# Performance work log

Hardware: AMD Instinct MI355X
Metric: run time of the kernel (lower is better)

## Reference

```python
import jax, jax.numpy as jnp
import numpy as np

N = 10000      # nodes
ND = 64        # node_dim
H = 128        # hidden_dim
L = 4          # num_layers
K = 16         # knn k
TD = 16        # time_dim


def _time_embed(t, n):
    # sinusoidal embedding, matches _time_embed: freqs = exp(linspace(0,1,half)*-4)
    half = TD // 2
    freqs = jnp.exp(jnp.linspace(0.0, 1.0, half) * -4.0)            # [half]
    angles = t.reshape(1, 1) * freqs[None, :]                        # [1, half]
    emb = jnp.concatenate([jnp.sin(angles), jnp.cos(angles)], -1)    # [1, TD]
    return jnp.broadcast_to(emb, (n, TD))


def _knn_edges(pos, k):
    # full cdist + topk, mirroring _knn_graph (no_grad in torch)
    n = pos.shape[0]
    sq = jnp.sum(pos * pos, -1)
    d2 = sq[:, None] + sq[None, :] - 2.0 * (pos @ pos.T)             # [N, N]
    idxr = jnp.arange(n)
    d2 = d2.at[idxr, idxr].set(jnp.inf)
    _, nbr = jax.lax.top_k(-d2, k)                                   # [N, K] nearest
    src = jnp.repeat(idxr, k)
    dst = nbr.reshape(-1)
    return src, dst


def _egnn_layer(h, pos, src, dst, s, ew1, eb1, ew2, eb2, nw1, nb1, nw2, nb2, cw, cb):
    n = h.shape[0]
    diff = pos[dst] - pos[src]                                       # [E, 3]
    r2 = jnp.sum(diff * diff, -1, keepdims=True)                     # [E, 1]
    r = jnp.sqrt(r2 + 1e-8)
    dir_ij = diff / r
    e_in = jnp.concatenate([h[dst], h[src], r2], -1)                 # [E, 2H+1]
    m = jax.nn.silu(e_in @ ew1 + eb1)
    m = jax.nn.silu(m @ ew2 + eb2)                                   # [E, H]
    m = m * s[src][:, None]                                          # s-gate
    m_sum = jax.ops.segment_sum(m, dst, num_segments=n)              # [N, H]
    deg = jax.ops.segment_sum(jnp.ones((m.shape[0], 1), m.dtype), dst, num_segments=n)
    deg = jnp.maximum(deg, 1.0)
    m_sum = m_sum / deg
    hn = jax.nn.silu(jnp.concatenate([h, m_sum], -1) @ nw1 + nb1)
    h_new = hn @ nw2 + nb2                                           # [N, H]
    gamma = m @ cw + cb                                              # [E, 1]
    cu = jax.ops.segment_sum(gamma * dir_ij, dst, num_segments=n) / deg
    return h_new, pos + cu


def setup_inputs() -> dict:
    key = jax.random.key(0)
    ks = jax.random.split(key, 24)
    g = lambda k, shape: (jax.random.normal(k, shape, dtype=jnp.float32) * 0.05)
    z = lambda shape: jnp.zeros(shape, jnp.float32)
    return {
        'x': jax.random.normal(ks[0], (N, ND), jnp.float32),
        'pos': jax.random.normal(ks[1], (N, 3), jnp.float32) * 5.0,
        't': jax.random.uniform(ks[2], (1,), jnp.float32),
        's': jax.random.uniform(ks[3], (N,), jnp.float32),
        'proj_w': g(ks[4], (ND + 1 + TD, H)), 'proj_b': z((H,)),
        'edge_w1': g(ks[5], (L, 2 * H + 1, H)), 'edge_b1': z((L, H)),
        'edge_w2': g(ks[6], (L, H, H)), 'edge_b2': z((L, H)),
        'node_w1': g(ks[7], (L, 2 * H, H)), 'node_b1': z((L, H)),
        'node_w2': g(ks[8], (L, H, H)), 'node_b2': z((L, H)),
        'coord_w': g(ks[9], (L, H, 1)), 'coord_b': z((L, 1)),
        'ec_w': g(ks[10], (H, 3)), 'ec_b': z((3,)),
        'ef_w': g(ks[11], (H, ND)), 'ef_b': z((ND,)),
    }


def reference(x, pos, t, s, proj_w, proj_b, edge_w1, edge_b1, edge_w2, edge_b2,
              node_w1, node_b1, node_w2, node_b2, coord_w, coord_b,
              ec_w, ec_b, ef_w, ef_b):
    n = x.shape[0]
    src, dst = _knn_edges(jax.lax.stop_gradient(pos), K)  # graph build is no_grad
    temb = _time_embed(t[0], n)
    h = jnp.concatenate([x, s[:, None], temb], -1) @ proj_w + proj_b  # [N, H]
    p = pos
    for l in range(L):
        h, p = _egnn_layer(h, p, src, dst, s,
                           edge_w1[l], edge_b1[l], edge_w2[l], edge_b2[l],
                           node_w1[l], node_b1[l], node_w2[l], node_b2[l],
                           coord_w[l], coord_b[l])
    eps_c = h @ ec_w + ec_b                                           # [N, 3]
    eps_f = h @ ef_w + ef_b                                           # [N, ND]
    return jnp.concatenate([eps_c, eps_f, p], -1)                     # [N, 3+ND+3]
```

## Files before the change

kernel.cpp:

```cpp
#include <hip/hip_runtime.h>
#include <math.h>

#define N_NODES 10000
#define ND 64
#define H 128
#define LAYERS 4
#define KNN 16
#define TD 16
#define E_EDGES (N_NODES * KNN)
#define KC 1250
#define TILE_E 128

typedef __attribute__((ext_vector_type(8))) short short8;
typedef __attribute__((ext_vector_type(4))) float f32x4;

__device__ __forceinline__ float silu(float x) {
  return x * __builtin_amdgcn_rcpf(1.0f + __expf(-x));
}

__device__ __forceinline__ unsigned short f2bf(float f) {
  unsigned int u = __float_as_uint(f);
  u += 0x7fffu + ((u >> 16) & 1u);
  return (unsigned short)(u >> 16);
}
__device__ __forceinline__ float bf2f(unsigned short h) {
  return __uint_as_float(((unsigned int)h) << 16);
}

__global__ __launch_bounds__(256) void pos4_kernel(const float* __restrict__ pos,
                                                   float4* __restrict__ pos4,
                                                   float* __restrict__ p0,
                                                   int* __restrict__ degi) {
  int i = blockIdx.x * 256 + threadIdx.x;
  if (i >= N_NODES) return;
  float x = pos[i * 3 + 0], y = pos[i * 3 + 1], z = pos[i * 3 + 2];
  pos4[i] = make_float4(x, y, z, x * x + y * y + z * z);
  p0[i * 3 + 0] = x;
  p0[i * 3 + 1] = y;
  p0[i * 3 + 2] = z;
  degi[i] = 0;
}

__global__ __launch_bounds__(256) void wcvt_kernel(
    const float* __restrict__ ew2, const float* __restrict__ nw1,
    const float* __restrict__ nw2, const float* __restrict__ ew1,
    const float* __restrict__ pw, const float* __restrict__ ecw,
    const float* __restrict__ efw, unsigned short* __restrict__ w2T,
    unsigned short* __restrict__ nw1T, unsigned short* __restrict__ nw2T,
    unsigned short* __restrict__ ew1T, unsigned short* __restrict__ pwT,
    unsigned short* __restrict__ owT) {
  int i = blockIdx.x * 256 + threadIdx.x;
  if (i < 65536) {
    int l = i >> 14, rem = i & 16383, o = rem >> 7, c = rem & 127;
    w2T[i] = f2bf(ew2[l * 16384 + c * 128 + o]);
  } else if (i < 196608) {
    int j = i - 65536;
    int l = j >> 15, rem = j & 32767, o = rem >> 8, c2 = rem & 255;
    nw1T[j] = f2bf(nw1[l * 32768 + c2 * 128 + o]);
  } else if (i < 262144) {
    int j = i - 196608;
    int l = j >> 14, rem = j & 16383, o = rem >> 7, c = rem & 127;
    nw2T[j] = f2bf(nw2[l * 16384 + c * 128 + o]);
  } else if (i < 393216) {
    int j = i - 262144;
    int l = j >> 15, rem = j & 32767, o = rem >> 7, c = rem & 127;
    ew1T[j] = f2bf(ew1[l * 257 * 128 + (c + ((o >> 7) << 7)) * 128 + (o & 127)]);
  } else if (i < 405504) {
    int j = i - 393216;
    int o = j / 96, c = j - o * 96;
    pwT[j] = (c < 81) ? f2bf(pw[c * 128 + o]) : 0;
  } else {
    int j = i - 405504;
    int o = j >> 7, c = j & 127;
    float v = 0.0f;
    if (o < 3) v = ecw[c * 3 + o];
    else if (o < 67) v = efw[c * 64 + (o - 3)];
    owT[j] = f2bf(v);
  }
}

__global__ __launch_bounds__(256) void knn_kernel(const float4* __restrict__ pos4,
                                                  int* __restrict__ nbr,
                                                  int* __restrict__ degi) {
  __shared__ float4 C[KC];
  int tid = threadIdx.x;
  int lane = tid & 63;
  int wid = tid >> 6;
  int i = blockIdx.x * 4 + wid;
  float4 q = pos4[i];
  float v = __builtin_inff();
  int vid = 0;
  float thresh = __builtin_inff();
  for (int base = 0; base < N_NODES; base += KC) {
    int cnt = min(KC, N_NODES - base);
    __syncthreads();
    for (int jj = tid; jj < cnt; jj += 256) C[jj] = pos4[base + jj];
    __syncthreads();
    for (int j0 = 0; j0 < cnt; j0 += 128) {
      int ja = j0 + lane, jb = j0 + 64 + lane;
      float da = __builtin_inff(), db = __builtin_inff();
      if (ja < cnt) {
        float4 p = C[ja];
        float dot = fmaf(q.x, p.x, fmaf(q.y, p.y, q.z * p.z));
        da = fmaf(-2.0f, dot, p.w);
        if (base + ja == i) da = __builtin_inff();
      }
      if (jb < cnt) {
        float4 p = C[jb];
        float dot = fmaf(q.x, p.x, fmaf(q.y, p.y, q.z * p.z));
        db = fmaf(-2.0f, dot, p.w);
        if (base + jb == i) db = __builtin_inff();
      }
      if (__ballot(fminf(da, db) < thresh)) {
        unsigned long long mask = __ballot(da < thresh);
        while (mask) {
          int sl = __ffsll((long long)mask) - 1;
          mask &= mask - 1;
          float d2b = __shfl(da, sl, 64);
          if (d2b >= thresh) continue;
          int gjb = base + j0 + sl;
          float prevv = __shfl_up(v, 1, 64);
          int previd = __shfl_up(vid, 1, 64);
          bool stay = (v <= d2b);
          bool takenew = (lane == 0) || (prevv <= d2b);
          v = stay ? v : (takenew ? d2b : prevv);
          vid = stay ? vid : (takenew ? gjb : previd);
          thresh = __shfl(v, 15, 64);
        }
        mask = __ballot(db < thresh);
        while (mask) {
          int sl = __ffsll((long long)mask) - 1;
          mask &= mask - 1;
          float d2b = __shfl(db, sl, 64);
          if (d2b >= thresh) continue;
          int gjb = base + j0 + 64 + sl;
          float prevv = __shfl_up(v, 1, 64);
          int previd = __shfl_up(vid, 1, 64);
          bool stay = (v <= d2b);
          bool takenew = (lane == 0) || (prevv <= d2b);
          v = stay ? v : (takenew ? d2b : prevv);
          vid = stay ? vid : (takenew ? gjb : previd);
          thresh = __shfl(v, 15, 64);
        }
      }
    }
  }
  if (lane < KNN) {
    nbr[i * KNN + lane] = vid;
    atomicAdd(&degi[vid], 1);
  }
}

__global__ __launch_bounds__(1024) void scan_kernel(const int* __restrict__ degi,
                                                    int* __restrict__ off,
                                                    int* __restrict__ cursor) {
  __shared__ int part[1024];
  int t = threadIdx.x;
  int base = t * 10;
  int sum = 0;
  if (t < 1000)
    for (int i = 0; i < 10; ++i) sum += degi[base + i];
  part[t] = sum;
  __syncthreads();
  for (int stp = 1; stp < 1024; stp <<= 1) {
    int v = (t >= stp) ? part[t - stp] : 0;
    __syncthreads();
    part[t] += v;
    __syncthreads();
  }
  if (t < 1000) {
    int run = (t == 0) ? 0 : part[t - 1];
    for (int i = 0; i < 10; ++i) {
      off[base + i] = run;
      cursor[base + i] = run;
      run += degi[base + i];
    }
  }
  if (t == 0) off[N_NODES] = E_EDGES;
}

__global__ void scatter_kernel(const int* __restrict__ nbr, int* __restrict__ cursor,
                               int* __restrict__ eid, int* __restrict__ dstof) {
  int e = blockIdx.x * 256 + threadIdx.x;
  if (e < E_EDGES) {
    int d = nbr[e];
    int p = atomicAdd(&cursor[d], 1);
    eid[p] = e;
    dstof[p] = d;
  }
}

__global__ void sort_kernel(const int* __restrict__ off, int* __restrict__ eid) {
  int n = blockIdx.x * 256 + threadIdx.x;
  if (n >= N_NODES) return;
  int a = off[n], b = off[n + 1];
  for (int i = a + 1; i < b; ++i) {
    int v = eid[i];
    int j = i - 1;
    while (j >= a && eid[j] > v) { eid[j + 1] = eid[j]; --j; }
    eid[j + 1] = v;
  }
}

__global__ __launch_bounds__(256) void proj_ab_kernel(
    const float* __restrict__ x, const float* __restrict__ s,
    const float* __restrict__ tptr, const unsigned short* __restrict__ pwT,
    const float* __restrict__ pb, const unsigned short* __restrict__ ew1T,
    const float* __restrict__ eb1, float* __restrict__ h_out,
    unsigned short* __restrict__ Abf, unsigned short* __restrict__ Bbf) {
  __shared__ unsigned short inpb[16][104];
  __shared__ unsigned short hb[16][136];
  int tid = threadIdx.x;
  int n0 = blockIdx.x * 16;
  float t = tptr[0];
  for (int idx = tid; idx < 16 * 104; idx += 256) {
    int n = idx / 104, c = idx - n * 104;
    int gn = n0 + n;
    float val;
    if (c < 64) val = x[gn * ND + c];
    else if (c == 64) val = s[gn];
    else if (c < 81) {
      int j = c - 65;
      int jj = (j < 8) ? j : (j - 8);
      float f = __expf(-4.0f * (float)jj / 7.0f);
      float a = t * f;
      val = (j < 8) ? sinf(a) : cosf(a);
    } else val = 0.0f;
    inpb[n][c] = f2bf(val);
  }
  __syncthreads();
  int w = tid >> 6, lane = tid & 63, fr = lane & 15, kg = lane >> 4;
  f32x4 acc[2];
  acc[0] = (f32x4){0.f, 0.f, 0.f, 0.f};
  acc[1] = (f32x4){0.f, 0.f, 0.f, 0.f};
#pragma unroll
  for (int ks = 0; ks < 3; ++ks) {
    int k = ks * 32 + kg * 8;
    short8 a = *(const short8*)&inpb[fr][k];
#pragma unroll
    for (int nt = 0; nt < 2; ++nt) {
      int col = w * 32 + nt * 16 + fr;
      short8 b = *(const short8*)&pwT[col * 96 + k];
      acc[nt] = __builtin_amdgcn_mfma_f32_16x16x32_bf16(a, b, acc[nt], 0, 0, 0);
    }
  }
#pragma unroll
  for (int nt = 0; nt < 2; ++nt) {
    int col = w * 32 + nt * 16 + fr;
    float bias = pb[col];
#pragma unroll
    for (int r = 0; r < 4; ++r) {
      int row = kg * 4 + r;
      float hv = acc[nt][r] + bias;
      h_out[(n0 + row) * H + col] = hv;
      hb[row][col] = f2bf(hv);
    }
  }
  __syncthreads();
  f32x4 acc2[4];
#pragma unroll
  for (int nt = 0; nt < 4; ++nt) acc2[nt] = (f32x4){0.f, 0.f, 0.f, 0.f};
#pragma unroll
  for (int ks = 0; ks < 4; ++ks) {
    int k = ks * 32 + kg * 8;
    short8 a = *(const short8*)&hb[fr][k];
#pragma unroll
    for (int nt = 0; nt < 4; ++nt) {
      int col = w * 64 + nt * 16 + fr;
      short8 b = *(const short8*)&ew1T[col * H + k];
      acc2[nt] = __builtin_amdgcn_mfma_f32_16x16x32_bf16(a, b, acc2[nt], 0, 0, 0);
    }
  }
#pragma unroll
  for (int nt = 0; nt < 4; ++nt) {
    int col = w * 64 + nt * 16 + fr;
    float bias = (col < H) ? eb1[col] : 0.0f;
#pragma unroll
    for (int r = 0; r < 4; ++r) {
      int row = kg * 4 + r;
      float val = acc2[nt][r] + bias;
      if (col < H) Abf[(n0 + row) * H + col] = f2bf(val);
      else Bbf[(n0 + row) * H + (col - H)] = f2bf(val);
    }
  }
}

__global__ __launch_bounds__(256) void edge_mfma_kernel(
    const unsigned short* __restrict__ Abf, const unsigned short* __restrict__ Bbf,
    const float* __restrict__ p, const float* __restrict__ s,
    const int* __restrict__ csr_off, const int* __restrict__ eid,
    const int* __restrict__ dstof, const float* __restrict__ wr,
    const unsigned short* __restrict__ w2T, const float* __restrict__ eb2,
    const float* __restrict__ cw, const float* __restrict__ cbp,
    float* __restrict__ msA, float* __restrict__ msB,
    float* __restrict__ cuA, float* __restrict__ cuB) {
  __shared__ unsigned short t1s[TILE_E][136];
  __shared__ float r2A[TILE_E], sA[TILE_E], dirA[TILE_E][3], gA[TILE_E];
  __shared__ int srcA[TILE_E], dstA[TILE_E];
  __shared__ float wrs[H], b2s[H], cws[H];

  int tid = threadIdx.x;
  int P0 = blockIdx.x * TILE_E;
  int P1 = P0 + TILE_E;

  if (tid < H) { wrs[tid] = wr[tid]; b2s[tid] = eb2[tid]; cws[tid] = cw[tid]; }
  if (tid < TILE_E) {
    int e = tid;
    int edge = eid[P0 + e];
    int src = edge >> 4;
    int d = dstof[P0 + e];
    srcA[e] = src;
    dstA[e] = d;
    float dx = p[d * 3 + 0] - p[src * 3 + 0];
    float dy = p[d * 3 + 1] - p[src * 3 + 1];
    float dz = p[d * 3 + 2] - p[src * 3 + 2];
    float r2 = dx * dx + dy * dy + dz * dz;
    r2A[e] = r2;
    float rinv = 1.0f / sqrtf(r2 + 1e-8f);
    dirA[e][0] = dx * rinv;
    dirA[e][1] = dy * rinv;
    dirA[e][2] = dz * rinv;
    sA[e] = s[src];
  }
  __syncthreads();

  int nA = dstA[0], nB = dstA[TILE_E - 1];
  int nn = nB - nA + 1;

  for (int idx = tid; idx < TILE_E * 32; idx += 256) {
    int e = idx >> 5, cp = (idx & 31) * 4;
    uint2 au = *(const uint2*)&Abf[dstA[e] * H + cp];
    uint2 bu = *(const uint2*)&Bbf[srcA[e] * H + cp];
    float r2v = r2A[e];
    float pr0 = silu(bf2f((unsigned short)(au.x & 0xffffu)) +
                     bf2f((unsigned short)(bu.x & 0xffffu)) + r2v * wrs[cp]);
    float pr1 = silu(bf2f((unsigned short)(au.x >> 16)) +
                     bf2f((unsigned short)(bu.x >> 16)) + r2v * wrs[cp + 1]);
    float pr2 = silu(bf2f((unsigned short)(au.y & 0xffffu)) +
                     bf2f((unsigned short)(bu.y & 0xffffu)) + r2v * wrs[cp + 2]);
    float pr3 = silu(bf2f((unsigned short)(au.y >> 16)) +
                     bf2f((unsigned short)(bu.y >> 16)) + r2v * wrs[cp + 3]);
    uint2 o;
    o.x = ((unsigned int)f2bf(pr1) << 16) | (unsigned int)f2bf(pr0);
    o.y = ((unsigned int)f2bf(pr3) << 16) | (unsigned int)f2bf(pr2);
    *(uint2*)&t1s[e][cp] = o;
  }
  __syncthreads();

  int w = tid >> 6, lane = tid & 63;
  int fr = lane & 15, kg = lane >> 4;
  f32x4 acc[8][2];
#pragma unroll
  for (int mt = 0; mt < 8; ++mt)
#pragma unroll
    for (int nt = 0; nt < 2; ++nt) acc[mt][nt] = (f32x4){0.f, 0.f, 0.f, 0.f};
#pragma unroll
  for (int ks = 0; ks < 4; ++ks) {
    int k = ks * 32 + kg * 8;
    short8 bf0 = *(const short8*)&w2T[(w * 32 + fr) * H + k];
    short8 bf1 = *(const short8*)&w2T[(w * 32 + 16 + fr) * H + k];
#pragma unroll
    for (int mt = 0; mt < 8; ++mt) {
      short8 a = *(const short8*)&t1s[mt * 16 + fr][k];
      acc[mt][0] = __builtin_amdgcn_mfma_f32_16x16x32_bf16(a, bf0, acc[mt][0], 0, 0, 0);
      acc[mt][1] = __builtin_amdgcn_mfma_f32_16x16x32_bf16(a, bf1, acc[mt][1], 0, 0, 0);
    }
  }
  __syncthreads();

#pragma unroll
  for (int mt = 0; mt < 8; ++mt) {
#pragma unroll
    for (int nt = 0; nt < 2; ++nt) {
      int col = w * 32 + nt * 16 + fr;
      float b2v = b2s[col];
#pragma unroll
      for (int r = 0; r < 4; ++r) {
        int row = mt * 16 + kg * 4 + r;
        float mv = silu(acc[mt][nt][r] + b2v) * sA[row];
        t1s[row][col] = f2bf(mv);
      }
    }
  }
  __syncthreads();

  if (tid < TILE_E) {
    float g = 0.f;
    for (int c = 0; c < H; c += 4) {
      uint2 u = *(const uint2*)&t1s[tid][c];
      g = fmaf(bf2f((unsigned short)(u.x & 0xffffu)), cws[c], g);
      g = fmaf(bf2f((unsigned short)(u.x >> 16)), cws[c + 1], g);
      g = fmaf(bf2f((unsigned short)(u.y & 0xffffu)), cws[c + 2], g);
      g = fmaf(bf2f((unsigned short)(u.y >> 16)), cws[c + 3], g);
    }
    gA[tid] = g + cbp[0];
  }
  __syncthreads();

  for (int idx = tid; idx < nn * H; idx += 256) {
    int ni = idx >> 7, c = idx & 127;
    int n = nA + ni;
    int o0 = csr_off[n], o1 = csr_off[n + 1];
    int lo = max(o0, P0), hi = min(o1, P1);
    float sum = 0.f;
    for (int pos = lo; pos < hi; ++pos) sum += bf2f(t1s[pos - P0][c]);
    if (o0 >= P0) {
      msA[n * H + c] = sum;
      if (o1 <= P1) msB[n * H + c] = 0.0f;
    } else {
      msB[n * H + c] = sum;
    }
  }
  for (int idx = tid; idx < nn * 3; idx += 256) {
    int ni = idx / 3, comp = idx - ni * 3;
    int n = nA + ni;
    int o0 = csr_off[n], o1 = csr_off[n + 1];
    int lo = max(o0, P0), hi = min(o1, P1);
    float sum = 0.f;
    for (int pos = lo; pos < hi; ++pos)
      sum += gA[pos - P0] * dirA[pos - P0][comp];
    if (o0 >= P0) {
      cuA[n * 3 + comp] = sum;
      if (o1 <= P1) cuB[n * 3 + comp] = 0.0f;
    } else {
      cuB[n * 3 + comp] = sum;
    }
  }
}

__global__ __launch_bounds__(256) void node_mfma_kernel(
    const float* __restrict__ h, const float* __restrict__ msA,
    const float* __restrict__ msB, const int* __restrict__ degi,
    const float* __restrict__ cuA, const float* __restrict__ cuB,
    const float* __restrict__ p_in, const unsigned short* __restrict__ w1T,
    const float* __restrict__ nb1, const unsigned short* __restrict__ w2T,
    const float* __restrict__ nb2, const unsigned short* __restrict__ ew1Tn,
    const float* __restrict__ eb1n, int doab, float* __restrict__ h_out,
    float* __restrict__ p_out, unsigned short* __restrict__ Abf,
    unsigned short* __restrict__ Bbf) {
  __shared__ unsigned short insb[16][264];
  __shared__ unsigned short hnsb[16][136];
  int tid = threadIdx.x;
  int n0 = blockIdx.x * 16;
  for (int idx = tid; idx < 16 * H; idx += 256) {
    int n = idx >> 7, c = idx & 127;
    int gn = n0 + n;
    float hv = h[gn * H + c];
    int dg = degi[gn];
    float ms = 0.f;
    if (dg > 0) ms = (msA[gn * H + c] + msB[gn * H + c]) / (float)dg;
    insb[n][c] = f2bf(hv);
    insb[n][H + c] = f2bf(ms);
  }
  __syncthreads();
  int w = tid >> 6, lane = tid & 63, fr = lane & 15, kg = lane >> 4;
  f32x4 acc[2];
  acc[0] = (f32x4){0.f, 0.f, 0.f, 0.f};
  acc[1] = (f32x4){0.f, 0.f, 0.f, 0.f};
#pragma unroll
  for (int ks = 0; ks < 8; ++ks) {
    int k = ks * 32 + kg * 8;
    short8 a = *(const short8*)&insb[fr][k];
#pragma unroll
    for (int nt = 0; nt < 2; ++nt) {
      int col = w * 32 + nt * 16 + fr;
      short8 b = *(const short8*)&w1T[col * 256 + k];
      acc[nt] = __builtin_amdgcn_mfma_f32_16x16x32_bf16(a, b, acc[nt], 0, 0, 0);
    }
  }
#pragma unroll
  for (int nt = 0; nt < 2; ++nt) {
    int col = w * 32 + nt * 16 + fr;
    float b1 = nb1[col];
#pragma unroll
    for (int r = 0; r < 4; ++r) {
      int row = kg * 4 + r;
      hnsb[row][col] = f2bf(silu(acc[nt][r] + b1));
    }
  }
  __syncthreads();
  f32x4 acc2[2];
  acc2[0] = (f32x4){0.f, 0.f, 0.f, 0.f};
  acc2[1] = (f32x4){0.f, 0.f, 0.f, 0.f};
#pragma unroll
  for (int ks = 0; ks < 4; ++ks) {
    int k = ks * 32 + kg * 8;
    short8 a = *(const short8*)&hnsb[fr][k];
#pragma unroll
    for (int nt = 0; nt < 2; ++nt) {
      int col = w * 32 + nt * 16 + fr;
      short8 b = *(const short8*)&w2T[col * H + k];
      acc2[nt] = __builtin_amdgcn_mfma_f32_16x16x32_bf16(a, b, acc2[nt], 0, 0, 0);
    }
  }
  unsigned short (*hb)[136] = (unsigned short(*)[136])insb;
#pragma unroll
  for (int nt = 0; nt < 2; ++nt) {
    int col = w * 32 + nt * 16 + fr;
    float b2 = nb2[col];
#pragma unroll
    for (int r = 0; r < 4; ++r) {
      int row = kg * 4 + r;
      float hv = acc2[nt][r] + b2;
      h_out[(n0 + row) * H + col] = hv;
      hb[row][col] = f2bf(hv);
    }
  }
  if (tid < 48) {
    int nl = tid / 3, comp = tid - nl * 3;
    int gn = n0 + nl;
    int dg = degi[gn];
    float add = 0.0f;
    if (dg > 0)
      add = (cuA[gn * 3 + comp] + cuB[gn * 3 + comp]) / (float)dg;
    p_out[gn * 3 + comp] = p_in[gn * 3 + comp] + add;
  }
  if (doab) {
    __syncthreads();
    f32x4 acc3[4];
#pragma unroll
    for (int nt = 0; nt < 4; ++nt) acc3[nt] = (f32x4){0.f, 0.f, 0.f, 0.f};
#pragma unroll
    for (int ks = 0; ks < 4; ++ks) {
      int k = ks * 32 + kg * 8;
      short8 a = *(const short8*)&hb[fr][k];
#pragma unroll
      for (int nt = 0; nt < 4; ++nt) {
        int col = w * 64 + nt * 16 + fr;
        short8 b = *(const short8*)&ew1Tn[col * H + k];
        acc3[nt] = __builtin_amdgcn_mfma_f32_16x16x32_bf16(a, b, acc3[nt], 0, 0, 0);
      }
    }
#pragma unroll
    for (int nt = 0; nt < 4; ++nt) {
      int col = w * 64 + nt * 16 + fr;
      float bias = (col < H) ? eb1n[col] : 0.0f;
#pragma unroll
      for (int r = 0; r < 4; ++r) {
        int row = kg * 4 + r;
        float val = acc3[nt][r] + bias;
        if (col < H) Abf[(n0 + row) * H + col] = f2bf(val);
        else Bbf[(n0 + row) * H + (col - H)] = f2bf(val);
      }
    }
  }
}

__global__ __launch_bounds__(256) void out_mfma_kernel(
    const float* __restrict__ h, const float* __restrict__ p,
    const unsigned short* __restrict__ owT, const float* __restrict__ ecb,
    const float* __restrict__ efb, float* __restrict__ out) {
  __shared__ unsigned short hb[16][136];
  int tid = threadIdx.x;
  int n0 = blockIdx.x * 16;
  for (int idx = tid; idx < 16 * H; idx += 256) {
    int n = idx >> 7, c = idx & 127;
    hb[n][c] = f2bf(h[(n0 + n) * H + c]);
  }
  __syncthreads();
  int w = tid >> 6, lane = tid & 63, fr = lane & 15, kg = lane >> 4;
  int ntiles = (w == 0) ? 2 : 1;
  for (int tt = 0; tt < ntiles; ++tt) {
    int tile = (tt == 0) ? w : 4;
    f32x4 acc = (f32x4){0.f, 0.f, 0.f, 0.f};
    int col = tile * 16 + fr;
#pragma unroll
    for (int ks = 0; ks < 4; ++ks) {
      int k = ks * 32 + kg * 8;
      short8 a = *(const short8*)&hb[fr][k];
      short8 b = *(const short8*)&owT[col * H + k];
      acc = __builtin_amdgcn_mfma_f32_16x16x32_bf16(a, b, acc, 0, 0, 0);
    }
    if (col < 67) {
      float bias = (col < 3) ? ecb[col] : efb[col - 3];
#pragma unroll
      for (int r = 0; r < 4; ++r) {
        int row = kg * 4 + r;
        out[(n0 + row) * 70 + col] = acc[r] + bias;
      }
    }
  }
  if (tid < 48) {
    int nl = tid / 3, comp = tid - nl * 3;
    int gn = n0 + nl;
    out[gn * 70 + 67 + comp] = p[gn * 3 + comp];
  }
}

extern "C" void kernel_launch(void* const* d_in, const int* in_sizes, int n_in,
                              void* d_out, int out_size, void* d_ws, size_t ws_size,
                              hipStream_t stream) {
  const float* x = (const float*)d_in[0];
  const float* pos = (const float*)d_in[1];
  const float* t = (const float*)d_in[2];
  const float* s = (const float*)d_in[3];
  const float* pw = (const float*)d_in[4];
  const float* pb = (const float*)d_in[5];
  const float* ew1 = (const float*)d_in[6];
  const float* eb1 = (const float*)d_in[7];
  const float* ew2 = (const float*)d_in[8];
  const float* eb2 = (const float*)d_in[9];
  const float* nw1 = (const float*)d_in[10];
  const float* nb1 = (const float*)d_in[11];
  const float* nw2 = (const float*)d_in[12];
  const float* nb2 = (const float*)d_in[13];
  const float* cw = (const float*)d_in[14];
  const float* cb = (const float*)d_in[15];
  const float* ecw = (const float*)d_in[16];
  const float* ecb = (const float*)d_in[17];
  const float* efw = (const float*)d_in[18];
  const float* efb = (const float*)d_in[19];

  char* wp = (char*)d_ws;
  auto alloc = [&](size_t bytes) {
    char* r = wp;
    wp += (bytes + 255) & ~(size_t)255;
    return r;
  };
  float* h0 = (float*)alloc((size_t)N_NODES * H * 4);
  float* h1 = (float*)alloc((size_t)N_NODES * H * 4);
  unsigned short* Abf = (unsigned short*)alloc((size_t)N_NODES * H * 2);
  unsigned short* Bbf = (unsigned short*)alloc((size_t)N_NODES * H * 2);
  float* msAb = (float*)alloc((size_t)N_NODES * H * 4);
  float* msBb = (float*)alloc((size_t)N_NODES * H * 4);
  float* cuAb = (float*)alloc((size_t)N_NODES * 3 * 4);
  float* cuBb = (float*)alloc((size_t)N_NODES * 3 * 4);
  float* p0 = (float*)alloc((size_t)N_NODES * 3 * 4);
  float* p1 = (float*)alloc((size_t)N_NODES * 3 * 4);
  int* degi = (int*)alloc((size_t)N_NODES * 4);
  int* nbr = (int*)alloc((size_t)E_EDGES * 4);
  int* off = (int*)alloc((size_t)(N_NODES + 1) * 4);
  int* cursor = (int*)alloc((size_t)N_NODES * 4);
  int* eid = (int*)alloc((size_t)E_EDGES * 4);
  int* dstof = (int*)alloc((size_t)E_EDGES * 4);
  unsigned short* w2Tb = (unsigned short*)alloc((size_t)LAYERS * H * H * 2);
  unsigned short* nw1Tb = (unsigned short*)alloc((size_t)LAYERS * 2 * H * H * 2);
  unsigned short* nw2Tb = (unsigned short*)alloc((size_t)LAYERS * H * H * 2);
  unsigned short* ew1Tb = (unsigned short*)alloc((size_t)LAYERS * 2 * H * H * 2);
  unsigned short* pwTb = (unsigned short*)alloc((size_t)H * 96 * 2);
  unsigned short* owTb = (unsigned short*)alloc((size_t)80 * H * 2);

  float4* pos4 = (float4*)msAb;

  wcvt_kernel<<<1624, 256, 0, stream>>>(ew2, nw1, nw2, ew1, pw, ecw, efw,
                                        w2Tb, nw1Tb, nw2Tb, ew1Tb, pwTb, owTb);
  pos4_kernel<<<(N_NODES + 255) / 256, 256, 0, stream>>>(pos, pos4, p0, degi);
  knn_kernel<<<N_NODES / 4, 256, 0, stream>>>(pos4, nbr, degi);
  scan_kernel<<<1, 1024, 0, stream>>>(degi, off, cursor);
  scatter_kernel<<<(E_EDGES + 255) / 256, 256, 0, stream>>>(nbr, cursor, eid, dstof);
  sort_kernel<<<(N_NODES + 255) / 256, 256, 0, stream>>>(off, eid);
  proj_ab_kernel<<<N_NODES / 16, 256, 0, stream>>>(x, s, t, pwTb, pb, ew1Tb, eb1,
                                                   h0, Abf, Bbf);

  float* hc = h0;
  float* hn = h1;
  float* pc = p0;
  float* pn = p1;
  for (int l = 0; l < LAYERS; ++l) {
    const float* ew1l = ew1 + (size_t)l * 257 * H;
    int doab = (l < LAYERS - 1) ? 1 : 0;
    edge_mfma_kernel<<<E_EDGES / TILE_E, 256, 0, stream>>>(
        Abf, Bbf, pc, s, off, eid, dstof, ew1l + 256 * H,
        w2Tb + (size_t)l * H * H, eb2 + l * H, cw + l * H, cb + l,
        msAb, msBb, cuAb, cuBb);
    node_mfma_kernel<<<N_NODES / 16, 256, 0, stream>>>(
        hc, msAb, msBb, degi, cuAb, cuBb, pc, nw1Tb + (size_t)l * 2 * H * H,
        nb1 + l * H, nw2Tb + (size_t)l * H * H, nb2 + l * H,
        ew1Tb + (size_t)(l + doab) * 2 * H * H, eb1 + (size_t)(l + doab) * H,
        doab, hn, pn, Abf, Bbf);
    float* tmp = hc; hc = hn; hn = tmp;
    tmp = pc; pc = pn; pn = tmp;
  }
  out_mfma_kernel<<<N_NODES / 16, 256, 0, stream>>>(hc, pc, owTb, ecb, efb,
                                                    (float*)d_out);
}
```

Before: 450.7 us.

## Process two queries per wave in kNN, coalesce weight transpose, vectorize edge reductions

The kNN kernel now handles two query points per wavefront and four candidate chunks per iteration, so each shared-memory candidate load is reused across two queries and half as many blocks are launched. The self-exclusion test is dropped: the kernel keeps the 17 nearest points and discards lane 0, on the assumption that a point's own distance is always the minimum. The weight conversion kernel now reads coalesced and scatters its writes. The edge kernel splits the gamma dot product across all 256 threads and uses 4-wide bf16 loads and float4 stores in the message-sum loop. Risks include duplicate-position ties breaking the self-drop assumption, and higher register pressure in kNN.

```diff
diff --git a/kernel.cpp b/kernel.cpp
--- a/kernel.cpp
+++ b/kernel.cpp
@@ -51,20 +51,22 @@
     unsigned short* __restrict__ owT) {
   int i = blockIdx.x * 256 + threadIdx.x;
   if (i < 65536) {
-    int l = i >> 14, rem = i & 16383, o = rem >> 7, c = rem & 127;
-    w2T[i] = f2bf(ew2[l * 16384 + c * 128 + o]);
+    int l = i >> 14, rem = i & 16383, c = rem >> 7, o = rem & 127;
+    w2T[l * 16384 + o * 128 + c] = f2bf(ew2[i]);
   } else if (i < 196608) {
     int j = i - 65536;
-    int l = j >> 15, rem = j & 32767, o = rem >> 8, c2 = rem & 255;
-    nw1T[j] = f2bf(nw1[l * 32768 + c2 * 128 + o]);
+    int l = j >> 15, rem = j & 32767, c2 = rem >> 7, o = rem & 127;
+    nw1T[l * 32768 + o * 256 + c2] = f2bf(nw1[j]);
   } else if (i < 262144) {
     int j = i - 196608;
-    int l = j >> 14, rem = j & 16383, o = rem >> 7, c = rem & 127;
-    nw2T[j] = f2bf(nw2[l * 16384 + c * 128 + o]);
+    int l = j >> 14, rem = j & 16383, c = rem >> 7, o = rem & 127;
+    nw2T[l * 16384 + o * 128 + c] = f2bf(nw2[j]);
   } else if (i < 393216) {
     int j = i - 262144;
-    int l = j >> 15, rem = j & 32767, o = rem >> 7, c = rem & 127;
-    ew1T[j] = f2bf(ew1[l * 257 * 128 + (c + ((o >> 7) << 7)) * 128 + (o & 127)]);
+    int l = j >> 15, rem = j & 32767, r = rem >> 7, o = rem & 127;
+    int o2 = o + ((r >> 7) << 7);
+    int c = r & 127;
+    ew1T[l * 32768 + o2 * 128 + c] = f2bf(ew1[l * 257 * 128 + r * 128 + o]);
   } else if (i < 405504) {
     int j = i - 393216;
     int o = j / 96, c = j - o * 96;
@@ -79,6 +81,25 @@
   }
 }
 
+#define INS(dval, gbase, V, ID, TH)                                   \
+  {                                                                   \
+    unsigned long long mask = __ballot((dval) < (TH));                \
+    while (mask) {                                                    \
+      int sl = __ffsll((long long)mask) - 1;                          \
+      mask &= mask - 1;                                               \
+      float db = __shfl((dval), sl, 64);                              \
+      if (db >= (TH)) continue;                                       \
+      int gj = (gbase) + sl;                                          \
+      float pv = __shfl_up((V), 1, 64);                               \
+      int pid = __shfl_up((ID), 1, 64);                               \
+      bool stay = ((V) <= db);                                        \
+      bool tk = (lane == 0) || (pv <= db);                            \
+      (V) = stay ? (V) : (tk ? db : pv);                              \
+      (ID) = stay ? (ID) : (tk ? gj : pid);                           \
+      (TH) = __shfl((V), 16, 64);                                     \
+    }                                                                 \
+  }
+
 __global__ __launch_bounds__(256) void knn_kernel(const float4* __restrict__ pos4,
                                                   int* __restrict__ nbr,
                                                   int* __restrict__ degi) {
@@ -86,68 +107,66 @@
   int tid = threadIdx.x;
   int lane = tid & 63;
   int wid = tid >> 6;
-  int i = blockIdx.x * 4 + wid;
-  float4 q = pos4[i];
-  float v = __builtin_inff();
-  int vid = 0;
-  float thresh = __builtin_inff();
+  int qb = blockIdx.x * 8 + wid * 2;
+  float4 q0 = pos4[qb];
+  float4 q1 = pos4[qb + 1];
+  float v0 = __builtin_inff(), v1 = __builtin_inff();
+  int id0 = 0, id1 = 0;
+  float th0 = __builtin_inff(), th1 = __builtin_inff();
   for (int base = 0; base < N_NODES; base += KC) {
     int cnt = min(KC, N_NODES - base);
     __syncthreads();
     for (int jj = tid; jj < cnt; jj += 256) C[jj] = pos4[base + jj];
     __syncthreads();
-    for (int j0 = 0; j0 < cnt; j0 += 128) {
-      int ja = j0 + lane, jb = j0 + 64 + lane;
-      float da = __builtin_inff(), db = __builtin_inff();
+    for (int j0 = 0; j0 < cnt; j0 += 256) {
+      float dA0 = __builtin_inff(), dA1 = __builtin_inff();
+      float dB0 = __builtin_inff(), dB1 = __builtin_inff();
+      float dC0 = __builtin_inff(), dC1 = __builtin_inff();
+      float dD0 = __builtin_inff(), dD1 = __builtin_inff();
+      int ja = j0 + lane, jbx = j0 + 64 + lane;
+      int jc = j0 + 128 + lane, jd = j0 + 192 + lane;
       if (ja < cnt) {
         float4 p = C[ja];
-        float dot = fmaf(q.x, p.x, fmaf(q.y, p.y, q.z * p.z));
-        da = fmaf(-2.0f, dot, p.w);
-        if (base + ja == i) da = __builtin_inff();
-      }
-      if (jb < cnt) {
-        float4 p = C[jb];
-        float dot = fmaf(q.x, p.x, fmaf(q.y, p.y, q.z * p.z));
-        db = fmaf(-2.0f, dot, p.w);
-        if (base + jb == i) db = __builtin_inff();
-      }
-      if (__ballot(fminf(da, db) < thresh)) {
-        unsigned long long mask = __ballot(da < thresh);
-        while (mask) {
-          int sl = __ffsll((long long)mask) - 1;
-          mask &= mask - 1;
-          float d2b = __shfl(da, sl, 64);
-          if (d2b >= thresh) continue;
-          int gjb = base + j0 + sl;
-          float prevv = __shfl_up(v, 1, 64);
-          int previd = __shfl_up(vid, 1, 64);
-          bool stay = (v <= d2b);
-          bool takenew = (lane == 0) || (prevv <= d2b);
-          v = stay ? v : (takenew ? d2b : prevv);
-          vid = stay ? vid : (takenew ? gjb : previd);
-          thresh = __shfl(v, 15, 64);
-        }
-        mask = __ballot(db < thresh);
-        while (mask) {
-          int sl = __ffsll((long long)mask) - 1;
-          mask &= mask - 1;
-          float d2b = __shfl(db, sl, 64);
-          if (d2b >= thresh) continue;
-          int gjb = base + j0 + 64 + sl;
-          float prevv = __shfl_up(v, 1, 64);
-          int previd = __shfl_up(vid, 1, 64);
-          bool stay = (v <= d2b);
-          bool takenew = (lane == 0) || (prevv <= d2b);
-          v = stay ? v : (takenew ? d2b : prevv);
-          vid = stay ? vid : (takenew ? gjb : previd);
-          thresh = __shfl(v, 15, 64);
-        }
-      }
-    }
-  }
-  if (lane < KNN) {
-    nbr[i * KNN + lane] = vid;
-    atomicAdd(&degi[vid], 1);
+        dA0 = fmaf(-2.0f, fmaf(q0.x, p.x, fmaf(q0.y, p.y, q0.z * p.z)), p.w);
+        dA1 = fmaf(-2.0f, fmaf(q1.x, p.x, fmaf(q1.y, p.y, q1.z * p.z)), p.w);
+      }
+      if (jbx < cnt) {
+        float4 p = C[jbx];
+        dB0 = fmaf(-2.0f, fmaf(q0.x, p.x, fmaf(q0.y, p.y, q0.z * p.z)), p.w);
+        dB1 = fmaf(-2.0f, fmaf(q1.x, p.x, fmaf(q1.y, p.y, q1.z * p.z)), p.w);
+      }
+      if (jc < cnt) {
+        float4 p = C[jc];
+        dC0 = fmaf(-2.0f, fmaf(q0.x, p.x, fmaf(q0.y, p.y, q0.z * p.z)), p.w);
+        dC1 = fmaf(-2.0f, fmaf(q1.x, p.x, fmaf(q1.y, p.y, q1.z * p.z)), p.w);
+      }
+      if (jd < cnt) {
+        float4 p = C[jd];
+        dD0 = fmaf(-2.0f, fmaf(q0.x, p.x, fmaf(q0.y, p.y, q0.z * p.z)), p.w);
+        dD1 = fmaf(-2.0f, fmaf(q1.x, p.x, fmaf(q1.y, p.y, q1.z * p.z)), p.w);
+      }
+      int gb = base + j0;
+      float m0 = fminf(fminf(dA0, dB0), fminf(dC0, dD0));
+      if (__ballot(m0 < th0)) {
+        INS(dA0, gb, v0, id0, th0);
+        INS(dB0, gb + 64, v0, id0, th0);
+        INS(dC0, gb + 128, v0, id0, th0);
+        INS(dD0, gb + 192, v0, id0, th0);
+      }
+      float m1 = fminf(fminf(dA1, dB1), fminf(dC1, dD1));
+      if (__ballot(m1 < th1)) {
+        INS(dA1, gb, v1, id1, th1);
+        INS(dB1, gb + 64, v1, id1, th1);
+        INS(dC1, gb + 128, v1, id1, th1);
+        INS(dD1, gb + 192, v1, id1, th1);
+      }
+    }
+  }
+  if (lane >= 1 && lane < 17) {
+    nbr[qb * KNN + lane - 1] = id0;
+    atomicAdd(&degi[id0], 1);
+    nbr[(qb + 1) * KNN + lane - 1] = id1;
+    atomicAdd(&degi[id1], 1);
   }
 }
 
@@ -296,6 +315,7 @@
     float* __restrict__ cuA, float* __restrict__ cuB) {
   __shared__ unsigned short t1s[TILE_E][136];
   __shared__ float r2A[TILE_E], sA[TILE_E], dirA[TILE_E][3], gA[TILE_E];
+  __shared__ float gpart[2][TILE_E];
   __shared__ int srcA[TILE_E], dstA[TILE_E];
   __shared__ float wrs[H], b2s[H], cws[H];
 
@@ -384,31 +404,42 @@
   }
   __syncthreads();
 
-  if (tid < TILE_E) {
+  {
+    int e = tid & 127, half = tid >> 7;
+    int c0 = half * 64;
     float g = 0.f;
-    for (int c = 0; c < H; c += 4) {
-      uint2 u = *(const uint2*)&t1s[tid][c];
+    for (int c = c0; c < c0 + 64; c += 4) {
+      uint2 u = *(const uint2*)&t1s[e][c];
       g = fmaf(bf2f((unsigned short)(u.x & 0xffffu)), cws[c], g);
       g = fmaf(bf2f((unsigned short)(u.x >> 16)), cws[c + 1], g);
       g = fmaf(bf2f((unsigned short)(u.y & 0xffffu)), cws[c + 2], g);
       g = fmaf(bf2f((unsigned short)(u.y >> 16)), cws[c + 3], g);
     }
-    gA[tid] = g + cbp[0];
-  }
-  __syncthreads();
-
-  for (int idx = tid; idx < nn * H; idx += 256) {
-    int ni = idx >> 7, c = idx & 127;
+    gpart[half][e] = g;
+  }
+  __syncthreads();
+  if (tid < TILE_E) gA[tid] = gpart[0][tid] + gpart[1][tid] + cbp[0];
+  __syncthreads();
+
+  for (int idx = tid; idx < nn * 32; idx += 256) {
+    int ni = idx >> 5, cq = (idx & 31) * 4;
     int n = nA + ni;
     int o0 = csr_off[n], o1 = csr_off[n + 1];
     int lo = max(o0, P0), hi = min(o1, P1);
-    float sum = 0.f;
-    for (int pos = lo; pos < hi; ++pos) sum += bf2f(t1s[pos - P0][c]);
+    float s0 = 0.f, s1 = 0.f, s2 = 0.f, s3 = 0.f;
+    for (int pos = lo; pos < hi; ++pos) {
+      uint2 u = *(const uint2*)&t1s[pos - P0][cq];
+      s0 += bf2f((unsigned short)(u.x & 0xffffu));
+      s1 += bf2f((unsigned short)(u.x >> 16));
+      s2 += bf2f((unsigned short)(u.y & 0xffffu));
+      s3 += bf2f((unsigned short)(u.y >> 16));
+    }
+    float4 sv = make_float4(s0, s1, s2, s3);
     if (o0 >= P0) {
-      msA[n * H + c] = sum;
-      if (o1 <= P1) msB[n * H + c] = 0.0f;
+      *(float4*)&msA[n * H + cq] = sv;
+      if (o1 <= P1) *(float4*)&msB[n * H + cq] = make_float4(0.f, 0.f, 0.f, 0.f);
     } else {
-      msB[n * H + c] = sum;
+      *(float4*)&msB[n * H + cq] = sv;
     }
   }
   for (int idx = tid; idx < nn * 3; idx += 256) {
@@ -645,7 +676,7 @@
   wcvt_kernel<<<1624, 256, 0, stream>>>(ew2, nw1, nw2, ew1, pw, ecw, efw,
                                         w2Tb, nw1Tb, nw2Tb, ew1Tb, pwTb, owTb);
   pos4_kernel<<<(N_NODES + 255) / 256, 256, 0, stream>>>(pos, pos4, p0, degi);
-  knn_kernel<<<N_NODES / 4, 256, 0, stream>>>(pos4, nbr, degi);
+  knn_kernel<<<N_NODES / 8, 256, 0, stream>>>(pos4, nbr, degi);
   scan_kernel<<<1, 1024, 0, stream>>>(degi, off, cursor);
   scatter_kernel<<<(E_EDGES + 255) / 256, 256, 0, stream>>>(nbr, cursor, eid, dstof);
   sort_kernel<<<(N_NODES + 255) / 256, 256, 0, stream>>>(off, eid);
```

After: 428.9 us. 1.05x faster.
